# Optimization experiments

Hardware: AMD Instinct MI355X
Metric: run time of the kernel (lower is better)

The kernel has to match this reference:

```python
import jax, jax.numpy as jnp
import numpy as np
from jax import lax

G = 64      # ngroup
CPN = 4     # channels per group in hidden layers
H, W = 32, 64
K = 5       # conv kernel
BIN = 8     # bin_num
BIAS = 3.5  # (bin_num-1)/2
NMIX = 3    # GMM components (batch replicas)
SCALE = 65536.0


def _group_mask(cout, cin, strict):
    # wavefront causality: tap (dg, di, dj) allowed iff dg+di+dj < 0 (strict) or <= 0
    g = jnp.arange(G)
    dg = g[None, :] - g[:, None]                      # (Gout, Gin)
    off = jnp.arange(K) - K // 2
    dd = off[:, None] + off[None, :]                  # (K, K)
    tot = dg[:, :, None, None] + dd[None, None, :, :]
    m = (tot < 0) if strict else (tot <= 0)
    m = jnp.repeat(jnp.repeat(m, cout, axis=0), cin, axis=1)
    return m.astype(jnp.float32)                      # (G*cout, G*cin, K, K)


def _cconv(x, w, b, m, relu):
    y = lax.conv_general_dilated(x, w * m, (1, 1), 'SAME',
                                 dimension_numbers=('NCHW', 'OIHW', 'NCHW'))
    y = y + b[None, :, None, None]
    return jax.nn.relu(y) if relu else y


def setup_inputs() -> dict:
    key = jax.random.key(0)
    ks = jax.random.split(key, 8)
    data = jax.random.randint(ks[0], (1, G, H, W), 0, BIN).astype(jnp.float32)
    mask = jax.random.randint(ks[1], (1, G, H, W), 0, 2).astype(jnp.float32)
    s = 0.05
    w_in = jax.random.normal(ks[2], (G * CPN, G, K, K), jnp.float32) * s
    b_in = jnp.zeros((G * CPN,), jnp.float32)
    w_hid = jax.random.normal(ks[3], (10, G * CPN, G * CPN, K, K), jnp.float32) * s
    b_hid = jnp.zeros((10, G * CPN), jnp.float32)
    w_out = jax.random.normal(ks[4], (G * NMIX, G * CPN, K, K), jnp.float32) * s
    b_out = jnp.zeros((G * NMIX,), jnp.float32)
    return dict(data=data, mask=mask, w_in=w_in, b_in=b_in,
                w_hid=w_hid, b_hid=b_hid, w_out=w_out, b_out=b_out)


def reference(data, mask, w_in, b_in, w_hid, b_hid, w_out, b_out):
    m_in = _group_mask(CPN, 1, True)      # first layer: strict (excludes current group)
    m_hid = _group_mask(CPN, CPN, False)
    m_out = _group_mask(NMIX, CPN, False)
    tdata = (data - BIAS) * mask
    x = jnp.concatenate([tdata, tdata, tdata], axis=0)   # (3, G, H, W)
    x = _cconv(x, w_in, b_in, m_in, True)
    for i in range(5):                                   # 5 residual blocks
        h = _cconv(x, w_hid[2 * i], b_hid[2 * i], m_hid, True)
        h = _cconv(h, w_hid[2 * i + 1], b_hid[2 * i + 1], m_hid, True)
        x = x + h
    y = _cconv(x, w_out, b_out, m_out, False)            # (3, G*3, H, W)
    y = y.reshape(NMIX, G, NMIX, H, W)                   # batch replica m -> mixture m
    logits = y[:, :, 0]
    mu = y[:, :, 1]
    sig = jax.nn.softplus(y[:, :, 2]) + 1e-6
    wts = jax.nn.softmax(logits, axis=0)                 # (3, G, H, W)
    edges = jnp.arange(BIN, dtype=jnp.float32) + 0.5 - BIAS
    z = (edges[:, None, None, None, None] - mu[None]) / (sig[None] * jnp.float32(np.sqrt(2.0)))
    cdf = 0.5 * (1.0 + lax.erf(z))                       # (BIN, 3, G, H, W)
    table = jnp.einsum('kmghw,mghw->ghwk', cdf, wts) * SCALE
    return table                                         # (G, H, W, BIN) quantizable CDF
```

## Files before the change

### kernel.cpp

```cpp
#include <hip/hip_runtime.h>
#include <math.h>

typedef _Float16 f16;
typedef _Float16 f16x8 __attribute__((ext_vector_type(8)));
typedef float f32x4 __attribute__((ext_vector_type(4)));

#define HH 32
#define WW 64
#define NPX 2048
#define SLOTS 68
#define CHS 78336
#define LOSCALE 2048.0f
#define INV_LOSCALE 4.8828125e-4f

typedef const __attribute__((address_space(1))) void gvoid;
typedef __attribute__((address_space(3))) void lvoid;
__device__ __forceinline__ void gload_lds16(const void* g, void* l) {
    __builtin_amdgcn_global_load_lds((gvoid*)g, (lvoid*)l, 16, 0, 0);
}

__device__ __forceinline__ void repack_tile(
    const float* __restrict__ W, f16* __restrict__ WP, float* RAWF,
    int Cin, int nCoT, int nCic, int cpg_in_log2, int limb, int is_out,
    int coT, int cic, int plane)
{
    const int nt = blockDim.x, t = threadIdx.x;
    const int co0 = coT * 16, ci0 = cic * 32;
    for (int u = t; u < 3200; u += nt) {
        int co16 = u / 200, j4 = u - co16 * 200;
        int co_p = co0 + co16;
        int co_orig = is_out ? 3 * (co_p >> 1) + 1 + (co_p & 1) : co_p;
        float4 v = *(const float4*)(W + (size_t)(co_orig * Cin + ci0) * 25 + j4 * 4);
        *(float4*)&RAWF[co16 * 800 + j4 * 4] = v;
    }
    __syncthreads();
    const int base = (coT * nCic + cic) * 512;
    const int tapStride = nCoT * nCic * 512;
    for (int e = t; e < 12800; e += nt) {
        int tap = e >> 9, r = e & 511;
        int co16 = r >> 5, ci32 = r & 31;
        int ky = tap / 5, kx = tap - 5 * ky;
        int co_p = co0 + co16;
        int g_out = is_out ? (co_p >> 1) : (co_p >> 2);
        int g_in = (ci0 + ci32) >> cpg_in_log2;
        float v = 0.f;
        if (ky + kx <= limb + g_out - g_in)
            v = RAWF[co16 * 800 + ci32 * 25 + tap];
        f16 vh = (f16)v;
        int dst = base + tap * tapStride + co16 * 32 + ci32;
        WP[dst] = vh;
        WP[plane + dst] = (f16)((v - (float)vh) * LOSCALE);
    }
}

__global__ __launch_bounds__(256) void init_kernel(
    const float* __restrict__ data, const float* __restrict__ mask,
    f16* __restrict__ PQ, f16* __restrict__ X0,
    const float* __restrict__ w_in, f16* __restrict__ WP)
{
    __shared__ __align__(16) float RAWF[12800];
    const int b = blockIdx.x, t = threadIdx.x;
    if (b < 1224) {
        *(int4*)(PQ + (size_t)(b * 256 + t) * 8) = make_int4(0, 0, 0, 0);
    } else if (b < 1836) {
        int e = (b - 1224) * 256 + t;
        int si = e >> 6, ci = e & 63;
        int row = si / 68, slot = si - row * 68;
        float v = 0.f;
        if (row >= 2 && row < 34 && slot >= 2 && slot < 66) {
            int px = (row - 2) * 64 + (slot - 2);
            v = (data[ci * NPX + px] - 3.5f) * mask[ci * NPX + px];
        }
        int dst = (ci >> 5) * CHS + si * 32 + (ci & 31);
        X0[dst] = (f16)v;
        X0[156672 + dst] = (f16)0.f;
    } else {
        int rb = b - 1836;
        repack_tile(w_in, WP, RAWF, 64, 16, 2, 0, 3, 0, rb >> 1, rb & 1, 409600);
    }
}

__global__ __launch_bounds__(320, 4) void conv_kernel(
    const f16* __restrict__ IN, int Cin, int inPlane,
    const f16* __restrict__ WP, int wPlane,
    const float* __restrict__ bias,
    const f16* __restrict__ RES, int resPlane,
    f16* __restrict__ OA, int oaPlane,
    float* __restrict__ OT,
    int nmt, int Coutp, int cpg_out, int cpg_in, int limb, int mode,
    const float* __restrict__ rW, f16* __restrict__ rWP,
    int rCin, int rnCoT, int rnCic, int rcpg_in_log2, int rlimb, int ris_out,
    int rplane, int nConv)
{
    __shared__ __align__(16) char SMEM[51200];
    f16* BL = (f16*)SMEM;
    float* RED = (float*)SMEM;

    if (blockIdx.x >= (unsigned)nConv) {
        int rb = blockIdx.x - nConv;
        repack_tile(rW, rWP, (float*)SMEM, rCin, rnCoT, rnCic,
                    rcpg_in_log2, rlimb, ris_out, rb / rnCic, rb % rnCic, rplane);
        return;
    }

    const int t = threadIdx.x;
    const int kw = t >> 6;
    const int lane = t & 63, l15 = lane & 15, q = lane >> 4;

    const int b = blockIdx.x;
    const int p3 = b & 7, r = b >> 3;
    int pairIdx, slot, h_;
    if (nmt == 16) { pairIdx = p3;     h_ = r & 31; slot = r >> 5; }
    else           { pairIdx = p3 & 3; h_ = r;      slot = p3 >> 2; }
    const int h = h_;
    const int mt = slot ? (nmt - 1 - pairIdx) : pairIdx;
    const int co0 = mt * 16;
    const int g_max = (co0 + 15) / cpg_out;

    int cnt[5];
#pragma unroll
    for (int kx = 0; kx < 5; kx++) {
        int c = (g_max + limb - (kw + kx) + 1) * cpg_in;
        c = c < Cin ? c : Cin;
        cnt[kx] = c > 0 ? c : 0;
    }
    int ci_top = (g_max + limb + 1) * cpg_in;
    ci_top = ci_top < Cin ? ci_top : Cin;
    const int NT = (ci_top + 31) >> 5;

    int soff[9];
    const int rowg = (h + kw) * 2176;
#pragma unroll
    for (int r9 = 0; r9 < 9; ++r9) {
        int u = r9 * 64 + lane;
        if (u > 543) u = 543;
        int pl = u >= 272 ? 1 : 0;
        int rem = u - (pl ? 272 : 0);
        soff[r9] = pl * inPlane + rowg + rem * 8;
    }
    f16* const wreg = BL + kw * 4608;

    f32x4 acc_h[4], acc_m[4];
#pragma unroll
    for (int j = 0; j < 4; j++) {
        acc_h[j] = (f32x4){0.f, 0.f, 0.f, 0.f};
        acc_m[j] = (f32x4){0.f, 0.f, 0.f, 0.f};
    }

    const size_t kxs = (size_t)Coutp * Cin;
    const f16* wb0 = WP + (size_t)(kw * 5 * (Coutp >> 4) + mt) * ((size_t)Cin << 4)
                   + l15 * 32 + q * 8;

#pragma unroll
    for (int r9 = 0; r9 < 9; ++r9)
        gload_lds16(IN + soff[r9], wreg + r9 * 512);

    for (int it = 0; it < NT; ++it) {
        const int ci0 = it << 5;
        const f16* wb = wb0 + it * 512;
        f16x8 cah, cal, nah, nal;
        if (ci0 < cnt[0]) {
            cah = *(const f16x8*)(wb);
            cal = *(const f16x8*)(wb + wPlane);
        }
        asm volatile("s_waitcnt vmcnt(0)" ::: "memory");

        const f16* bhp = wreg + q * 8;
        const f16* blp = bhp + 2176;
#pragma unroll
        for (int kx = 0; kx < 5; kx++) {
            if (ci0 >= cnt[kx]) break;
            if (kx < 4 && ci0 < cnt[kx + 1]) {
                nah = *(const f16x8*)(wb + (kx + 1) * kxs);
                nal = *(const f16x8*)(wb + (kx + 1) * kxs + wPlane);
            }
#pragma unroll
            for (int j = 0; j < 4; j++) {
                int slt = j * 16 + l15 + kx;
                f16x8 bh = *(const f16x8*)(bhp + slt * 32);
                f16x8 bl = *(const f16x8*)(blp + slt * 32);
                acc_h[j] = __builtin_amdgcn_mfma_f32_16x16x32_f16(cah, bh, acc_h[j], 0, 0, 0);
                acc_m[j] = __builtin_amdgcn_mfma_f32_16x16x32_f16(cah, bl, acc_m[j], 0, 0, 0);
                acc_m[j] = __builtin_amdgcn_mfma_f32_16x16x32_f16(cal, bh, acc_m[j], 0, 0, 0);
            }
            cah = nah; cal = nal;
        }
        if (it + 1 < NT) {
            asm volatile("s_waitcnt lgkmcnt(0)" ::: "memory");
            const int coff = (it + 1) * CHS;
#pragma unroll
            for (int r9 = 0; r9 < 9; ++r9)
                gload_lds16(IN + soff[r9] + coff, wreg + r9 * 512);
        }
    }

    __syncthreads();
#pragma unroll
    for (int j = 0; j < 4; j++) {
        f32x4 v;
#pragma unroll
        for (int rr = 0; rr < 4; rr++)
            v[rr] = acc_h[j][rr] + acc_m[j][rr] * INV_LOSCALE;
        *(f32x4*)&RED[(kw * 64 + j * 16 + l15) * 20 + q * 4] = v;
    }
    __syncthreads();

    if (mode == 0) {
        for (int c = t; c < 1024; c += 320) {
            int px = c >> 4, col = c & 15;
            float v = bias[co0 + col];
#pragma unroll
            for (int k5 = 0; k5 < 5; k5++) v += RED[(k5 * 64 + px) * 20 + col];
            v = fmaxf(v, 0.f);
            int cc = co0 + col;
            int o = (cc >> 5) * CHS + ((h + 2) * SLOTS + px + 2) * 32 + (cc & 31);
            if (RES) v += (float)RES[o] + (float)RES[resPlane + o] * INV_LOSCALE;
            f16 vh = (f16)v;
            OA[o] = vh;
            OA[oaPlane + o] = (f16)((v - (float)vh) * LOSCALE);
        }
    } else {
        for (int c = t; c < 1024; c += 320) {
            int px = c >> 4, col = c & 15;
            float v = bias[3 * ((co0 + col) >> 1) + 1 + (col & 1)];
#pragma unroll
            for (int k5 = 0; k5 < 5; k5++) v += RED[(k5 * 64 + px) * 20 + col];
            RED[px * 20 + col] = v;
        }
        __syncthreads();
        for (int c = t; c < 512; c += 320) {
            int px = c >> 3, gl = c & 7;
            float mu = RED[px * 20 + 2 * gl];
            float s  = RED[px * 20 + 2 * gl + 1];
            float sp = fmaxf(s, 0.f) + log1pf(expf(-fabsf(s)));
            float sig = sp + 1e-6f;
            float inv = 1.f / (sig * 1.41421356237f);
            int g = (co0 >> 1) + gl;
            float* o = OT + ((size_t)g * NPX + h * WW + px) * 8;
#pragma unroll
            for (int k = 0; k < 8; k++) {
                float z = ((float)k - 3.0f - mu) * inv;
                o[k] = 32768.f * (1.f + erff(z));
            }
        }
    }
}

extern "C" void kernel_launch(void* const* d_in, const int* in_sizes, int n_in,
                              void* d_out, int out_size, void* d_ws, size_t ws_size,
                              hipStream_t stream) {
    const float* data  = (const float*)d_in[0];
    const float* mask  = (const float*)d_in[1];
    const float* w_in  = (const float*)d_in[2];
    const float* b_in  = (const float*)d_in[3];
    const float* w_hid = (const float*)d_in[4];
    const float* b_hid = (const float*)d_in[5];
    const float* w_out = (const float*)d_in[6];
    const float* b_out = (const float*)d_in[7];
    float* out = (float*)d_out;

    f16* WPA = (f16*)d_ws;
    f16* WPB = WPA + 3276800;
    f16* P   = WPB + 3276800;
    f16* Q   = P + 1253376;
    f16* X0  = Q + 1253376;

    init_kernel<<<1868, 256, 0, stream>>>(data, mask, P, X0, w_in, WPA);

    f16* cur = WPA;
    f16* nxt = WPB;

    conv_kernel<<<640, 320, 0, stream>>>(X0, 64, 156672, cur, 409600,
        b_in, nullptr, 0, P, 626688, nullptr, 16, 256, 4, 1, 3, 0,
        w_hid, nxt, 256, 16, 8, 2, 4, 0, 1638400, 512);
    { f16* tmp = cur; cur = nxt; nxt = tmp; }

    for (int k = 1; k <= 10; ++k) {
        const int isLast = (k == 10);
        const float* rw = isLast ? w_out : (w_hid + (size_t)k * 1638400);
        const int rgrid = isLast ? 64 : 128;
        const int rnCoT = isLast ? 8 : 16;
        const int ris   = isLast ? 1 : 0;
        const int rpl   = isLast ? 819200 : 1638400;
        if (k & 1)
            conv_kernel<<<512 + rgrid, 320, 0, stream>>>(P, 256, 626688, cur, 1638400,
                b_hid + (size_t)(k - 1) * 256, nullptr, 0, Q, 626688, nullptr,
                16, 256, 4, 4, 4, 0,
                rw, nxt, 256, rnCoT, 8, 2, 4, ris, rpl, 512);
        else
            conv_kernel<<<512 + rgrid, 320, 0, stream>>>(Q, 256, 626688, cur, 1638400,
                b_hid + (size_t)(k - 1) * 256, P, 626688, P, 626688, nullptr,
                16, 256, 4, 4, 4, 0,
                rw, nxt, 256, rnCoT, 8, 2, 4, ris, rpl, 512);
        f16* tmp = cur; cur = nxt; nxt = tmp;
    }

    conv_kernel<<<256, 320, 0, stream>>>(P, 256, 626688, cur, 819200,
        b_out, nullptr, 0, nullptr, 0, out, 8, 128, 2, 4, 4, 1,
        nullptr, nullptr, 256, 8, 1, 2, 4, 0, 0, 256);
}
```

Measured before the change: 429.2 us.

## Software-pipeline LDS B-fragment loads against MFMAs with register double buffering

Unrolls the kx loop of the conv kernel by hand and double-buffers both the A weight fragments and the B activation fragments. Fragments for the next tap are read from LDS while the current tap's MFMAs run, and the last tap's MFMAs are moved after the next channel chunk's global-to-LDS prefetch is issued. The wait before the first tap now lets the two just-issued weight loads stay outstanding, and MFMA groups are wrapped in s_setprio. The aim is to hide LDS and global latency behind matrix work. In exchange register pressure rises, and launch bounds drop from 4 to 3 waves per SIMD to make room, which lowers occupancy.

```diff
diff --git a/kernel.cpp b/kernel.cpp
--- a/kernel.cpp
+++ b/kernel.cpp
@@ -80,7 +80,30 @@
     }
 }
 
-__global__ __launch_bounds__(320, 4) void conv_kernel(
+#define LOADB(BH, BL, KX)                                   \
+    BH##0 = *(const f16x8*)(bhp + (l15 + (KX)) * 32);       \
+    BH##1 = *(const f16x8*)(bhp + (l15 + (KX) + 16) * 32);  \
+    BH##2 = *(const f16x8*)(bhp + (l15 + (KX) + 32) * 32);  \
+    BH##3 = *(const f16x8*)(bhp + (l15 + (KX) + 48) * 32);  \
+    BL##0 = *(const f16x8*)(blp + (l15 + (KX)) * 32);       \
+    BL##1 = *(const f16x8*)(blp + (l15 + (KX) + 16) * 32);  \
+    BL##2 = *(const f16x8*)(blp + (l15 + (KX) + 32) * 32);  \
+    BL##3 = *(const f16x8*)(blp + (l15 + (KX) + 48) * 32);
+
+#define MFMA3(AH, AL, BH, BL, J)                                                    \
+    acc_h[J] = __builtin_amdgcn_mfma_f32_16x16x32_f16(AH, BH, acc_h[J], 0, 0, 0);   \
+    acc_m[J] = __builtin_amdgcn_mfma_f32_16x16x32_f16(AH, BL, acc_m[J], 0, 0, 0);   \
+    acc_m[J] = __builtin_amdgcn_mfma_f32_16x16x32_f16(AL, BH, acc_m[J], 0, 0, 0);
+
+#define MFMAS(AH, AL, BH, BL)            \
+    __builtin_amdgcn_s_setprio(1);       \
+    MFMA3(AH, AL, BH##0, BL##0, 0)       \
+    MFMA3(AH, AL, BH##1, BL##1, 1)       \
+    MFMA3(AH, AL, BH##2, BL##2, 2)       \
+    MFMA3(AH, AL, BH##3, BL##3, 3)       \
+    __builtin_amdgcn_s_setprio(0);
+
+__global__ __launch_bounds__(320, 3) void conv_kernel(
     const f16* __restrict__ IN, int Cin, int inPlane,
     const f16* __restrict__ WP, int wPlane,
     const float* __restrict__ bias,
@@ -155,36 +178,45 @@
     for (int r9 = 0; r9 < 9; ++r9)
         gload_lds16(IN + soff[r9], wreg + r9 * 512);
 
+    const f16* bhp = wreg + q * 8;
+    const f16* blp = bhp + 2176;
+
     for (int it = 0; it < NT; ++it) {
         const int ci0 = it << 5;
         const f16* wb = wb0 + it * 512;
-        f16x8 cah, cal, nah, nal;
-        if (ci0 < cnt[0]) {
-            cah = *(const f16x8*)(wb);
-            cal = *(const f16x8*)(wb + wPlane);
-        }
-        asm volatile("s_waitcnt vmcnt(0)" ::: "memory");
-
-        const f16* bhp = wreg + q * 8;
-        const f16* blp = bhp + 2176;
-#pragma unroll
-        for (int kx = 0; kx < 5; kx++) {
-            if (ci0 >= cnt[kx]) break;
-            if (kx < 4 && ci0 < cnt[kx + 1]) {
-                nah = *(const f16x8*)(wb + (kx + 1) * kxs);
-                nal = *(const f16x8*)(wb + (kx + 1) * kxs + wPlane);
-            }
-#pragma unroll
-            for (int j = 0; j < 4; j++) {
-                int slt = j * 16 + l15 + kx;
-                f16x8 bh = *(const f16x8*)(bhp + slt * 32);
-                f16x8 bl = *(const f16x8*)(blp + slt * 32);
-                acc_h[j] = __builtin_amdgcn_mfma_f32_16x16x32_f16(cah, bh, acc_h[j], 0, 0, 0);
-                acc_m[j] = __builtin_amdgcn_mfma_f32_16x16x32_f16(cah, bl, acc_m[j], 0, 0, 0);
-                acc_m[j] = __builtin_amdgcn_mfma_f32_16x16x32_f16(cal, bh, acc_m[j], 0, 0, 0);
-            }
-            cah = nah; cal = nal;
-        }
+        f16x8 a0h, a0l, a1h, a1l;
+        f16x8 b0h0, b0h1, b0h2, b0h3, b0l0, b0l1, b0l2, b0l3;
+        f16x8 b1h0, b1h1, b1h2, b1h3, b1l0, b1l1, b1l2, b1l3;
+
+        a0h = *(const f16x8*)(wb);
+        a0l = *(const f16x8*)(wb + wPlane);
+        asm volatile("s_waitcnt vmcnt(2)" ::: "memory");
+
+        if (ci0 < cnt[0]) { LOADB(b0h, b0l, 0) }
+        if (ci0 < cnt[1]) {
+            a1h = *(const f16x8*)(wb + kxs);
+            a1l = *(const f16x8*)(wb + kxs + wPlane);
+            LOADB(b1h, b1l, 1)
+        }
+        if (ci0 < cnt[0]) { MFMAS(a0h, a0l, b0h, b0l) }
+        if (ci0 < cnt[2]) {
+            a0h = *(const f16x8*)(wb + 2 * kxs);
+            a0l = *(const f16x8*)(wb + 2 * kxs + wPlane);
+            LOADB(b0h, b0l, 2)
+        }
+        if (ci0 < cnt[1]) { MFMAS(a1h, a1l, b1h, b1l) }
+        if (ci0 < cnt[3]) {
+            a1h = *(const f16x8*)(wb + 3 * kxs);
+            a1l = *(const f16x8*)(wb + 3 * kxs + wPlane);
+            LOADB(b1h, b1l, 3)
+        }
+        if (ci0 < cnt[2]) { MFMAS(a0h, a0l, b0h, b0l) }
+        if (ci0 < cnt[4]) {
+            a0h = *(const f16x8*)(wb + 4 * kxs);
+            a0l = *(const f16x8*)(wb + 4 * kxs + wPlane);
+            LOADB(b0h, b0l, 4)
+        }
+        if (ci0 < cnt[3]) { MFMAS(a1h, a1l, b1h, b1l) }
         if (it + 1 < NT) {
             asm volatile("s_waitcnt lgkmcnt(0)" ::: "memory");
             const int coff = (it + 1) * CHS;
@@ -192,6 +224,7 @@
             for (int r9 = 0; r9 < 9; ++r9)
                 gload_lds16(IN + soff[r9] + coff, wreg + r9 * 512);
         }
+        if (ci0 < cnt[4]) { MFMAS(a0h, a0l, b0h, b0l) }
     }
 
     __syncthreads();
```

After: 555.7 us. 1.29x slower.
